# Performance work log

Measured on AMD Instinct MI355X. Metric: run time of the kernel, lower is better.

The kernel has to match this reference:

```python
import jax, jax.numpy as jnp
import numpy as np

NUM_EMBED = 1024
HEAD_SIZE = 64
B, T = 4, 4096

def setup_inputs() -> dict:
    key = jax.random.key(0)
    kx, kq, kk, kv = jax.random.split(key, 4)
    scale = NUM_EMBED ** -0.5
    return {
        "x": jax.random.normal(kx, (B, T, NUM_EMBED), dtype=jnp.float32),
        "Wq": jax.random.normal(kq, (NUM_EMBED, HEAD_SIZE), dtype=jnp.float32) * scale,
        "Wk": jax.random.normal(kk, (NUM_EMBED, HEAD_SIZE), dtype=jnp.float32) * scale,
        "Wv": jax.random.normal(kv, (NUM_EMBED, HEAD_SIZE), dtype=jnp.float32) * scale,
    }

def reference(x, Wq, Wk, Wv):
    # x: [B,T,C]; Wq/Wk/Wv: [C,H]
    q = jnp.einsum('btc,ch->bth', x, Wq)
    k = jnp.einsum('btc,ch->bth', x, Wk)
    v = jnp.einsum('btc,ch->bth', x, Wv)
    Tq = x.shape[1]
    att = jnp.einsum('bth,bsh->bts', q, k) * (k.shape[-1] ** -0.5)  # [B,T,T]
    causal = jnp.tril(jnp.ones((Tq, Tq), dtype=bool))
    att = jnp.where(causal, att, -jnp.inf)
    att = jax.nn.softmax(att, axis=-1)
    # dropout p=0 (eval mode): identity
    out = jnp.einsum('bts,bsh->bth', att, v)  # [B,T,H]
    return out
```

## Files before the change

kernel.cpp:

```cpp
#include <hip/hip_runtime.h>

#define B_ 4
#define T_ 4096
#define C_ 1024
#define H_ 64

typedef _Float16 half8  __attribute__((ext_vector_type(8)));
typedef _Float16 half4_ __attribute__((ext_vector_type(4)));
typedef float    floatx4 __attribute__((ext_vector_type(4)));

#define MFMA16(a, b, c)  __builtin_amdgcn_mfma_f32_16x16x32_f16(a, b, c, 0, 0, 0)
#define MFMA16K(a, b, c) __builtin_amdgcn_mfma_f32_16x16x16f16(a, b, c, 0, 0, 0)
#define LO4(v) __builtin_shufflevector(v, v, 0, 1, 2, 3)
#define HI4(v) __builtin_shufflevector(v, v, 4, 5, 6, 7)

__global__ __launch_bounds__(256) void pack_w_kn(
    const float* __restrict__ Wq, const float* __restrict__ Wk,
    const float* __restrict__ Wv, _Float16* __restrict__ Wt2)
{
    const int idx  = blockIdx.x * 256 + threadIdx.x;
    const int mt   = idx >> 14;
    const int j    = (idx >> 10) & 15;
    const int f    = (idx >> 9) & 1;
    const int lane = (idx >> 3) & 63;
    const int jj   = idx & 7;
    const int q = lane >> 4, c = lane & 15;
    const int k  = j * 64 + f * 32 + q * 8 + jj;
    const int hp = mt * 16 + c;
    const float* W = (hp < 64) ? Wq : (hp < 128) ? Wk : Wv;
    Wt2[idx] = (_Float16)W[k * H_ + (hp & 63)];
}

__global__ __launch_bounds__(512) void qkv_kn(
    const float* __restrict__ x, const _Float16* __restrict__ Wt2,
    _Float16* __restrict__ Qh, _Float16* __restrict__ Kpk,
    _Float16* __restrict__ Vpk)
{
    __shared__ _Float16 xs[2][32][72];
    const int tid  = threadIdx.x;
    const int lane = tid & 63, w = tid >> 6;
    const int q    = lane >> 4, c = lane & 15;
    const int nt   = w & 1;
    const int mg   = w >> 1;
    const int row0 = blockIdx.x * 32;

    const int srow = tid >> 4, scol = (tid & 15) * 4;
    const float* xg = x + (size_t)(row0 + srow) * C_ + scol;

    floatx4 acc[3];
    #pragma unroll
    for (int i = 0; i < 3; ++i) acc[i] = floatx4{0.f, 0.f, 0.f, 0.f};

    float4 g = *(const float4*)xg;

    for (int j = 0; j < 16; ++j) {
        half4_ hv;
        hv[0] = (_Float16)g.x; hv[1] = (_Float16)g.y;
        hv[2] = (_Float16)g.z; hv[3] = (_Float16)g.w;
        *(half4_*)(&xs[j & 1][srow][scol]) = hv;
        __syncthreads();
        if (j < 15) g = *(const float4*)(xg + (j + 1) * 64);

        const _Float16* xrow = &xs[j & 1][nt * 16 + c][q * 8];
        const half8 b0 = *(const half8*)xrow;
        const half8 b1 = *(const half8*)(xrow + 32);

        half8 a[6];
        #pragma unroll
        for (int i = 0; i < 3; ++i) {
            const size_t fb = ((size_t)((mg * 3 + i) * 16 + j) * 2) * 512 + lane * 8;
            a[i * 2]     = *(const half8*)(Wt2 + fb);
            a[i * 2 + 1] = *(const half8*)(Wt2 + fb + 512);
        }
        #pragma unroll
        for (int i = 0; i < 3; ++i) {
            acc[i] = MFMA16(a[i * 2],     b0, acc[i]);
            acc[i] = MFMA16(a[i * 2 + 1], b1, acc[i]);
        }
    }

    const int row = row0 + nt * 16 + c;
    const int b = row >> 12, t4 = row & (T_ - 1);
    const int kt = t4 >> 6;
    const size_t tbase = ((size_t)b * 64 + kt) * 4096;
    const int mtk = (t4 >> 4) & 3;
    const int kk  = t4 & 63;

    #pragma unroll
    for (int i = 0; i < 3; ++i) {
        const int gi = mg * 3 + i;
        if (gi < 4) {
            half4_ v;
            #pragma unroll
            for (int r = 0; r < 4; ++r) v[r] = (_Float16)acc[i][r];
            *(half4_*)(Qh + (size_t)row * H_ + gi * 16 + q * 4) = v;
        } else if (gi < 8) {
            half4_ v;
            #pragma unroll
            for (int r = 0; r < 4; ++r) v[r] = (_Float16)acc[i][r];
            const int e  = gi - 4;
            const int f  = e >> 1;
            const int qa = (e * 2 + (q >> 1)) & 3;
            *(half4_*)(Kpk + tbase + ((size_t)(mtk * 2 + f) * 64 + qa * 16 + c) * 8
                       + (q & 1) * 4) = v;
        } else {
            const int mtv = gi - 8;
            const int qa2 = (kk >> 2) & 3;
            const int h4  = (kk >> 4) & 1;
            const int f2  = kk >> 5;
            const int i2  = kk & 3;
            #pragma unroll
            for (int r = 0; r < 4; ++r) {
                const int cv = q * 4 + r;
                Vpk[tbase + ((size_t)(mtv * 2 + f2) * 64 + qa2 * 16 + cv) * 8
                    + h4 * 4 + i2] = (_Float16)acc[i][r];
            }
        }
    }
}

__global__ __launch_bounds__(512, 4) void attn_kn(
    const _Float16* __restrict__ Qh, const _Float16* __restrict__ Kpk,
    const _Float16* __restrict__ Vpk, float* __restrict__ out)
{
    __shared__ __align__(16) char smem[36864];
    const int lane = threadIdx.x & 63;
    const int w    = threadIdx.x >> 6;
    const int q    = lane >> 4, c = lane & 15;

    const int bid  = blockIdx.x;
    const int xcd  = bid & 7;
    const int slot = bid >> 3;
    const int b    = xcd >> 1;
    const int e    = xcd & 1;
    const int t32  = (slot < 32) ? (127 - (2 * slot + e))
                                 : (2 * (slot - 32) + e);

    const int row0 = t32 * 32;
    const int grow = b * T_ + row0;
    const int nk   = (t32 >> 1) + 1;

    const _Float16 qs = (_Float16)0.18033688f;
    half8 bq0[2], bq1[2];
    #pragma unroll
    for (int g = 0; g < 2; ++g) {
        const _Float16* qb = Qh + (size_t)(grow + g * 16 + c) * H_;
        bq0[g] = *(const half8*)(qb + q * 8);
        bq1[g] = *(const half8*)(qb + 32 + q * 8);
        bq0[g] *= qs; bq1[g] *= qs;
    }

    floatx4 o[4][2];
    #pragma unroll
    for (int i = 0; i < 4; ++i)
        #pragma unroll
        for (int g = 0; g < 2; ++g) o[i][g] = floatx4{0.f, 0.f, 0.f, 0.f};
    float m[2] = {-3.0e38f, -3.0e38f}, l[2] = {0.f, 0.f};

    for (int kt = w; kt < nk; kt += 8) {
        const int kb = kt * 64;
        const _Float16* Kt = Kpk + ((size_t)b * 64 + kt) * 4096;
        const _Float16* Vt = Vpk + ((size_t)b * 64 + kt) * 4096;
        half8 a0[4], a1[4];

        #pragma unroll
        for (int mt = 0; mt < 4; ++mt) {
            a0[mt] = *(const half8*)(Kt + ((size_t)(mt * 2)     * 64 + lane) * 8);
            a1[mt] = *(const half8*)(Kt + ((size_t)(mt * 2 + 1) * 64 + lane) * 8);
        }
        floatx4 s[4][2];
        #pragma unroll
        for (int mt = 0; mt < 4; ++mt)
            #pragma unroll
            for (int g = 0; g < 2; ++g) {
                floatx4 z = floatx4{0.f, 0.f, 0.f, 0.f};
                z = MFMA16(a0[mt], bq0[g], z);
                s[mt][g] = MFMA16(a1[mt], bq1[g], z);
            }
        #pragma unroll
        for (int mt = 0; mt < 4; ++mt) {
            a0[mt] = *(const half8*)(Vt + ((size_t)(mt * 2)     * 64 + lane) * 8);
            a1[mt] = *(const half8*)(Vt + ((size_t)(mt * 2 + 1) * 64 + lane) * 8);
        }

        if (kt == nk - 1) {
            #pragma unroll
            for (int mt = 0; mt < 4; ++mt)
                #pragma unroll
                for (int g = 0; g < 2; ++g)
                    #pragma unroll
                    for (int r = 0; r < 4; ++r)
                        if (kb + mt * 16 + q * 4 + r > row0 + g * 16 + c)
                            s[mt][g][r] = -3.0e38f;
        }

        half4_ ph[2][4];
        #pragma unroll
        for (int g = 0; g < 2; ++g) {
            float mx = s[0][g][0];
            #pragma unroll
            for (int mt = 0; mt < 4; ++mt)
                #pragma unroll
                for (int r = 0; r < 4; ++r) mx = fmaxf(mx, s[mt][g][r]);
            mx = fmaxf(mx, __shfl_xor(mx, 16, 64));
            mx = fmaxf(mx, __shfl_xor(mx, 32, 64));
            const float mn    = fmaxf(m[g], mx);
            const float alpha = exp2f(m[g] - mn);
            float sl = 0.f;
            #pragma unroll
            for (int mt = 0; mt < 4; ++mt)
                #pragma unroll
                for (int r = 0; r < 4; ++r) {
                    const float ev = exp2f(s[mt][g][r] - mn);
                    sl += ev;
                    ph[g][mt][r] = (_Float16)ev;
                }
            sl += __shfl_xor(sl, 16, 64);
            sl += __shfl_xor(sl, 32, 64);
            l[g] = l[g] * alpha + sl;
            m[g] = mn;
            #pragma unroll
            for (int mt = 0; mt < 4; ++mt) o[mt][g] *= alpha;
        }

        #pragma unroll
        for (int mt = 0; mt < 4; ++mt) {
            const half4_ v0 = LO4(a0[mt]);
            const half4_ v1 = HI4(a0[mt]);
            const half4_ v2 = LO4(a1[mt]);
            const half4_ v3 = HI4(a1[mt]);
            #pragma unroll
            for (int g = 0; g < 2; ++g) {
                o[mt][g] = MFMA16K(v0, ph[g][0], o[mt][g]);
                o[mt][g] = MFMA16K(v1, ph[g][1], o[mt][g]);
                o[mt][g] = MFMA16K(v2, ph[g][2], o[mt][g]);
                o[mt][g] = MFMA16K(v3, ph[g][3], o[mt][g]);
            }
        }
    }

    float* Ol = (float*)smem;
    float* Ml = (float*)(smem + 34816);
    float* Ll = (float*)(smem + 35840);
    __syncthreads();
    if (q == 0) { Ml[w * 32 + c] = m[0]; Ml[w * 32 + 16 + c] = m[1]; }
    __syncthreads();
    float M0 = Ml[c], M1 = Ml[16 + c];
    #pragma unroll
    for (int w2 = 1; w2 < 8; ++w2) {
        M0 = fmaxf(M0, Ml[w2 * 32 + c]);
        M1 = fmaxf(M1, Ml[w2 * 32 + 16 + c]);
    }
    const float alpha0 = exp2f(m[0] - M0);
    const float alpha1 = exp2f(m[1] - M1);
    if (q == 0) { Ll[w * 32 + c] = l[0] * alpha0; Ll[w * 32 + 16 + c] = l[1] * alpha1; }

    const int h0 = w * 8 + q * 2;
    #pragma unroll
    for (int gp = 0; gp < 2; ++gp) {
        const float a = gp ? alpha1 : alpha0;
        #pragma unroll
        for (int mt = 0; mt < 4; ++mt)
            #pragma unroll
            for (int r = 0; r < 4; ++r)
                Ol[w * 1088 + (mt * 16 + q * 4 + r) * 17 + c] = o[mt][gp][r] * a;
        __syncthreads();
        float L = 0.f;
        #pragma unroll
        for (int w2 = 0; w2 < 8; ++w2) L += Ll[w2 * 32 + gp * 16 + c];
        const float inv = 1.f / L;
        float ox = 0.f, oy = 0.f;
        #pragma unroll
        for (int w2 = 0; w2 < 8; ++w2) {
            ox += Ol[w2 * 1088 + h0 * 17 + c];
            oy += Ol[w2 * 1088 + (h0 + 1) * 17 + c];
        }
        float2 st; st.x = ox * inv; st.y = oy * inv;
        *(float2*)(out + (size_t)(grow + gp * 16 + c) * H_ + h0) = st;
        if (gp == 0) __syncthreads();
    }
}

extern "C" void kernel_launch(void* const* d_in, const int* in_sizes, int n_in,
                              void* d_out, int out_size, void* d_ws, size_t ws_size,
                              hipStream_t stream) {
    const float* x  = (const float*)d_in[0];
    const float* Wq = (const float*)d_in[1];
    const float* Wk = (const float*)d_in[2];
    const float* Wv = (const float*)d_in[3];
    float* out = (float*)d_out;

    _Float16* ws = (_Float16*)d_ws;
    _Float16* Wt2 = ws;
    _Float16* Qh  = ws + 196608;
    _Float16* Kpk = Qh + 1048576;
    _Float16* Vpk = Kpk + 1048576;

    hipLaunchKernelGGL(pack_w_kn, dim3(768), dim3(256), 0, stream, Wq, Wk, Wv, Wt2);
    hipLaunchKernelGGL(qkv_kn, dim3((B_ * T_) / 32), dim3(512), 0, stream,
                       x, Wt2, Qh, Kpk, Vpk);
    hipLaunchKernelGGL(attn_kn, dim3(512), dim3(512), 0, stream,
                       Qh, Kpk, Vpk, out);
}
```

Before: 165.5 us.

## Halve attention waves, prefetch K tiles, lazy rescale, vectorize weight packing

The attention kernel now runs 4 waves per block instead of 8, with a 256-thread launch and a smaller LDS reduction buffer. Each wave prefetches the next K tile into registers while the current tile is processed, and MFMA sections are wrapped in s_setprio. The online softmax skips the max update and rescale unless the new max exceeds the old one by more than 8, which trades some fp16 headroom for fewer exp/multiply ops. The weight packing kernel writes half8 vectors per thread and launches 8x fewer blocks, and the epilogue is rewritten with float4 stores.

```diff
diff --git a/kernel.cpp b/kernel.cpp
--- a/kernel.cpp
+++ b/kernel.cpp
@@ -18,17 +18,20 @@
     const float* __restrict__ Wq, const float* __restrict__ Wk,
     const float* __restrict__ Wv, _Float16* __restrict__ Wt2)
 {
-    const int idx  = blockIdx.x * 256 + threadIdx.x;
-    const int mt   = idx >> 14;
-    const int j    = (idx >> 10) & 15;
-    const int f    = (idx >> 9) & 1;
-    const int lane = (idx >> 3) & 63;
-    const int jj   = idx & 7;
+    const int base = (blockIdx.x * 256 + threadIdx.x) * 8;
+    const int mt   = base >> 14;
+    const int j    = (base >> 10) & 15;
+    const int f    = (base >> 9) & 1;
+    const int lane = (base >> 3) & 63;
     const int q = lane >> 4, c = lane & 15;
-    const int k  = j * 64 + f * 32 + q * 8 + jj;
+    const int k0 = j * 64 + f * 32 + q * 8;
     const int hp = mt * 16 + c;
     const float* W = (hp < 64) ? Wq : (hp < 128) ? Wk : Wv;
-    Wt2[idx] = (_Float16)W[k * H_ + (hp & 63)];
+    const float* src = W + k0 * H_ + (hp & 63);
+    half8 v;
+    #pragma unroll
+    for (int jj = 0; jj < 8; ++jj) v[jj] = (_Float16)src[jj * H_];
+    *(half8*)(Wt2 + base) = v;
 }
 
 __global__ __launch_bounds__(512) void qkv_kn(
@@ -119,13 +122,14 @@
     }
 }
 
-__global__ __launch_bounds__(512, 4) void attn_kn(
+__global__ __launch_bounds__(256, 3) void attn_kn(
     const _Float16* __restrict__ Qh, const _Float16* __restrict__ Kpk,
     const _Float16* __restrict__ Vpk, float* __restrict__ out)
 {
-    __shared__ __align__(16) char smem[36864];
-    const int lane = threadIdx.x & 63;
-    const int w    = threadIdx.x >> 6;
+    __shared__ __align__(16) char smem[18432];
+    const int tid  = threadIdx.x;
+    const int lane = tid & 63;
+    const int w    = tid >> 6;
     const int q    = lane >> 4, c = lane & 15;
 
     const int bid  = blockIdx.x;
@@ -135,7 +139,6 @@
     const int e    = xcd & 1;
     const int t32  = (slot < 32) ? (127 - (2 * slot + e))
                                  : (2 * (slot - 32) + e);
-
     const int row0 = t32 * 32;
     const int grow = b * T_ + row0;
     const int nk   = (t32 >> 1) + 1;
@@ -157,30 +160,48 @@
         for (int g = 0; g < 2; ++g) o[i][g] = floatx4{0.f, 0.f, 0.f, 0.f};
     float m[2] = {-3.0e38f, -3.0e38f}, l[2] = {0.f, 0.f};
 
-    for (int kt = w; kt < nk; kt += 8) {
+    const _Float16* Kb = Kpk + (size_t)b * 262144;
+    const _Float16* Vb = Vpk + (size_t)b * 262144;
+
+    half8 k0[4], k1[4], v0[4], v1[4];
+    {
+        const _Float16* Kt = Kb + (size_t)w * 4096;
+        #pragma unroll
+        for (int mt = 0; mt < 4; ++mt) {
+            k0[mt] = *(const half8*)(Kt + ((mt * 2)     * 64 + lane) * 8);
+            k1[mt] = *(const half8*)(Kt + ((mt * 2 + 1) * 64 + lane) * 8);
+        }
+    }
+
+    #pragma unroll 1
+    for (int kt = w; kt < nk; kt += 4) {
         const int kb = kt * 64;
-        const _Float16* Kt = Kpk + ((size_t)b * 64 + kt) * 4096;
-        const _Float16* Vt = Vpk + ((size_t)b * 64 + kt) * 4096;
-        half8 a0[4], a1[4];
-
-        #pragma unroll
-        for (int mt = 0; mt < 4; ++mt) {
-            a0[mt] = *(const half8*)(Kt + ((size_t)(mt * 2)     * 64 + lane) * 8);
-            a1[mt] = *(const half8*)(Kt + ((size_t)(mt * 2 + 1) * 64 + lane) * 8);
-        }
+
         floatx4 s[4][2];
+        __builtin_amdgcn_s_setprio(1);
         #pragma unroll
         for (int mt = 0; mt < 4; ++mt)
             #pragma unroll
             for (int g = 0; g < 2; ++g) {
                 floatx4 z = floatx4{0.f, 0.f, 0.f, 0.f};
-                z = MFMA16(a0[mt], bq0[g], z);
-                s[mt][g] = MFMA16(a1[mt], bq1[g], z);
-            }
+                z = MFMA16(k0[mt], bq0[g], z);
+                s[mt][g] = MFMA16(k1[mt], bq1[g], z);
+            }
+        __builtin_amdgcn_s_setprio(0);
+
+        const _Float16* Vt = Vb + (size_t)kt * 4096;
         #pragma unroll
         for (int mt = 0; mt < 4; ++mt) {
-            a0[mt] = *(const half8*)(Vt + ((size_t)(mt * 2)     * 64 + lane) * 8);
-            a1[mt] = *(const half8*)(Vt + ((size_t)(mt * 2 + 1) * 64 + lane) * 8);
+            v0[mt] = *(const half8*)(Vt + ((mt * 2)     * 64 + lane) * 8);
+            v1[mt] = *(const half8*)(Vt + ((mt * 2 + 1) * 64 + lane) * 8);
+        }
+        if (kt + 4 < nk) {
+            const _Float16* Kt = Kb + (size_t)(kt + 4) * 4096;
+            #pragma unroll
+            for (int mt = 0; mt < 4; ++mt) {
+                k0[mt] = *(const half8*)(Kt + ((mt * 2)     * 64 + lane) * 8);
+                k1[mt] = *(const half8*)(Kt + ((mt * 2 + 1) * 64 + lane) * 8);
+            }
         }
 
         if (kt == nk - 1) {
@@ -204,50 +225,54 @@
                 for (int r = 0; r < 4; ++r) mx = fmaxf(mx, s[mt][g][r]);
             mx = fmaxf(mx, __shfl_xor(mx, 16, 64));
             mx = fmaxf(mx, __shfl_xor(mx, 32, 64));
-            const float mn    = fmaxf(m[g], mx);
-            const float alpha = exp2f(m[g] - mn);
+            if (!__all(mx <= m[g] + 8.f)) {
+                const float mn    = fmaxf(m[g], mx);
+                const float alpha = exp2f(m[g] - mn);
+                l[g] *= alpha;
+                #pragma unroll
+                for (int mt = 0; mt < 4; ++mt) o[mt][g] *= alpha;
+                m[g] = mn;
+            }
             float sl = 0.f;
             #pragma unroll
             for (int mt = 0; mt < 4; ++mt)
                 #pragma unroll
                 for (int r = 0; r < 4; ++r) {
-                    const float ev = exp2f(s[mt][g][r] - mn);
+                    const float ev = exp2f(s[mt][g][r] - m[g]);
                     sl += ev;
                     ph[g][mt][r] = (_Float16)ev;
                 }
             sl += __shfl_xor(sl, 16, 64);
             sl += __shfl_xor(sl, 32, 64);
-            l[g] = l[g] * alpha + sl;
-            m[g] = mn;
-            #pragma unroll
-            for (int mt = 0; mt < 4; ++mt) o[mt][g] *= alpha;
-        }
-
+            l[g] += sl;
+        }
+
+        __builtin_amdgcn_s_setprio(1);
         #pragma unroll
         for (int mt = 0; mt < 4; ++mt) {
-            const half4_ v0 = LO4(a0[mt]);
-            const half4_ v1 = HI4(a0[mt]);
-            const half4_ v2 = LO4(a1[mt]);
-            const half4_ v3 = HI4(a1[mt]);
+            const half4_ va = LO4(v0[mt]);
+            const half4_ vb = HI4(v0[mt]);
+            const half4_ vc = LO4(v1[mt]);
+            const half4_ vd = HI4(v1[mt]);
             #pragma unroll
             for (int g = 0; g < 2; ++g) {
-                o[mt][g] = MFMA16K(v0, ph[g][0], o[mt][g]);
-                o[mt][g] = MFMA16K(v1, ph[g][1], o[mt][g]);
-                o[mt][g] = MFMA16K(v2, ph[g][2], o[mt][g]);
-                o[mt][g] = MFMA16K(v3, ph[g][3], o[mt][g]);
-            }
-        }
+                o[mt][g] = MFMA16K(va, ph[g][0], o[mt][g]);
+                o[mt][g] = MFMA16K(vb, ph[g][1], o[mt][g]);
+                o[mt][g] = MFMA16K(vc, ph[g][2], o[mt][g]);
+                o[mt][g] = MFMA16K(vd, ph[g][3], o[mt][g]);
+            }
+        }
+        __builtin_amdgcn_s_setprio(0);
     }
 
     float* Ol = (float*)smem;
-    float* Ml = (float*)(smem + 34816);
-    float* Ll = (float*)(smem + 35840);
-    __syncthreads();
+    float* Ml = (float*)(smem + 17408);
+    float* Ll = (float*)(smem + 17920);
     if (q == 0) { Ml[w * 32 + c] = m[0]; Ml[w * 32 + 16 + c] = m[1]; }
     __syncthreads();
     float M0 = Ml[c], M1 = Ml[16 + c];
     #pragma unroll
-    for (int w2 = 1; w2 < 8; ++w2) {
+    for (int w2 = 1; w2 < 4; ++w2) {
         M0 = fmaxf(M0, Ml[w2 * 32 + c]);
         M1 = fmaxf(M1, Ml[w2 * 32 + 16 + c]);
     }
@@ -255,7 +280,8 @@
     const float alpha1 = exp2f(m[1] - M1);
     if (q == 0) { Ll[w * 32 + c] = l[0] * alpha0; Ll[w * 32 + 16 + c] = l[1] * alpha1; }
 
-    const int h0 = w * 8 + q * 2;
+    const int c2 = tid >> 4;
+    const int h0 = (tid & 15) * 4;
     #pragma unroll
     for (int gp = 0; gp < 2; ++gp) {
         const float a = gp ? alpha1 : alpha0;
@@ -267,17 +293,17 @@
         __syncthreads();
         float L = 0.f;
         #pragma unroll
-        for (int w2 = 0; w2 < 8; ++w2) L += Ll[w2 * 32 + gp * 16 + c];
+        for (int w2 = 0; w2 < 4; ++w2) L += Ll[w2 * 32 + gp * 16 + c2];
         const float inv = 1.f / L;
-        float ox = 0.f, oy = 0.f;
-        #pragma unroll
-        for (int w2 = 0; w2 < 8; ++w2) {
-            ox += Ol[w2 * 1088 + h0 * 17 + c];
-            oy += Ol[w2 * 1088 + (h0 + 1) * 17 + c];
-        }
-        float2 st; st.x = ox * inv; st.y = oy * inv;
-        *(float2*)(out + (size_t)(grow + gp * 16 + c) * H_ + h0) = st;
-        if (gp == 0) __syncthreads();
+        floatx4 st = floatx4{0.f, 0.f, 0.f, 0.f};
+        #pragma unroll
+        for (int w2 = 0; w2 < 4; ++w2)
+            #pragma unroll
+            for (int r = 0; r < 4; ++r)
+                st[r] += Ol[w2 * 1088 + (h0 + r) * 17 + c2];
+        st *= inv;
+        *(floatx4*)(out + (size_t)(grow + gp * 16 + c2) * H_ + h0) = st;
+        __syncthreads();
     }
 }
 
@@ -296,9 +322,9 @@
     _Float16* Kpk = Qh + 1048576;
     _Float16* Vpk = Kpk + 1048576;
 
-    hipLaunchKernelGGL(pack_w_kn, dim3(768), dim3(256), 0, stream, Wq, Wk, Wv, Wt2);
+    hipLaunchKernelGGL(pack_w_kn, dim3(96), dim3(256), 0, stream, Wq, Wk, Wv, Wt2);
     hipLaunchKernelGGL(qkv_kn, dim3((B_ * T_) / 32), dim3(512), 0, stream,
                        x, Wt2, Qh, Kpk, Vpk);
-    hipLaunchKernelGGL(attn_kn, dim3(512), dim3(512), 0, stream,
+    hipLaunchKernelGGL(attn_kn, dim3(512), dim3(256), 0, stream,
                        Qh, Kpk, Vpk, out);
 }
```

New measurement: 145.8 us. 11.9% less time.
